# Kernel tuning notes

Hardware: AMD Instinct MI355X
Metric: run time of the kernel (lower is better)

## Reference

```python
import jax, jax.numpy as jnp
import numpy as np

N, M = 2048, 2048
NODE_DIM = 64
HIDDEN_DIM = 64  # must equal NODE_DIM due to broadcast in msg = weights * h_r
LN_EPS = 1e-5


def setup_inputs() -> dict:
    key = jax.random.key(0)
    ks = jax.random.split(key, 14)
    s_edge1 = 1.0 / np.sqrt(4.0)
    s_edge2 = 1.0 / np.sqrt(HIDDEN_DIM)
    s_n1 = 1.0 / np.sqrt(NODE_DIM + HIDDEN_DIM)
    s_n2 = 1.0 / np.sqrt(NODE_DIM)
    return {
        "h_l": jax.random.normal(ks[0], (N, NODE_DIM), jnp.float32),
        "x_l": jax.random.normal(ks[1], (N, 3), jnp.float32),
        "h_r": jax.random.normal(ks[2], (M, NODE_DIM), jnp.float32),
        "x_r": jax.random.normal(ks[3], (M, 3), jnp.float32),
        # edge_mlp: Linear(4, hidden), SiLU, Linear(hidden, hidden)
        "W1": jax.random.uniform(ks[4], (4, HIDDEN_DIM), jnp.float32, -s_edge1, s_edge1),
        "b1": jax.random.uniform(ks[5], (HIDDEN_DIM,), jnp.float32, -s_edge1, s_edge1),
        "W2": jax.random.uniform(ks[6], (HIDDEN_DIM, HIDDEN_DIM), jnp.float32, -s_edge2, s_edge2),
        "b2": jax.random.uniform(ks[7], (HIDDEN_DIM,), jnp.float32, -s_edge2, s_edge2),
        # node_update: Linear(node+hidden, node), LayerNorm(node), SiLU, Linear(node, node)
        "Wn1": jax.random.uniform(ks[8], (NODE_DIM + HIDDEN_DIM, NODE_DIM), jnp.float32, -s_n1, s_n1),
        "bn1": jax.random.uniform(ks[9], (NODE_DIM,), jnp.float32, -s_n1, s_n1),
        "ln_g": jnp.ones((NODE_DIM,), jnp.float32),
        "ln_b": jnp.zeros((NODE_DIM,), jnp.float32),
        "Wn2": jax.random.uniform(ks[10], (NODE_DIM, NODE_DIM), jnp.float32, -s_n2, s_n2),
        "bn2": jax.random.uniform(ks[11], (NODE_DIM,), jnp.float32, -s_n2, s_n2),
    }


def _forward(h_l, x_l, h_r, x_r, W1, b1, W2, b2, Wn1, bn1, ln_g, ln_b, Wn2, bn2):
    # squared pairwise distances [N, M]
    d2 = jnp.sum((x_l[:, None, :] - x_r[None, :, :]) ** 2, axis=-1)
    dist_feat = jnp.exp(-d2 / 5.0)
    # chemical-property interaction matrices from last 3 node features
    l_p, r_p = h_l[:, -3:], h_r[:, -3:]
    hbond = l_p[:, 0:1] * r_p[:, 1:2].T + l_p[:, 1:2] * r_p[:, 0:1].T  # [N, M]
    hydro = l_p[:, 2:3] * r_p[:, 2:3].T                                # [N, M]
    edge_raw = jnp.stack([dist_feat, hbond, hydro, jnp.ones_like(d2)], axis=-1)  # [N, M, 4]
    # edge MLP -> sigmoid gating weights [N, M, H]
    e = jax.nn.silu(edge_raw @ W1 + b1) @ W2 + b2
    w = jax.nn.sigmoid(e)
    # weighted, normalized aggregation over M
    h_agg = jnp.einsum('nmh,mh->nh', w, h_r) / (jnp.sum(w, axis=1) + 1e-6)
    # node update MLP with LayerNorm
    z = jnp.concatenate([h_l, h_agg], axis=-1) @ Wn1 + bn1
    mu = jnp.mean(z, axis=-1, keepdims=True)
    var = jnp.var(z, axis=-1, keepdims=True)
    z = (z - mu) / jnp.sqrt(var + LN_EPS) * ln_g + ln_b
    z = jax.nn.silu(z) @ Wn2 + bn2
    return h_l + z


def reference(h_l, x_l, h_r, x_r, W1, b1, W2, b2, Wn1, bn1, ln_g, ln_b, Wn2, bn2):
    return _forward(h_l, x_l, h_r, x_r, W1, b1, W2, b2, Wn1, bn1, ln_g, ln_b, Wn2, bn2)
```

## Files before the change

kernel.cpp:

```cpp
#include <hip/hip_runtime.h>
#include <hip/hip_bf16.h>
#include <hip/hip_fp16.h>


#define NTOT 2048
#define MTOT 2048
#define MSPLIT 32
#define MCHUNK 64
#define NODE_ROWS 4

typedef _Float16 f16x8 __attribute__((ext_vector_type(8)));
typedef float f32x4  __attribute__((ext_vector_type(4)));
typedef float f32x2  __attribute__((ext_vector_type(2)));
typedef int   i32x4  __attribute__((ext_vector_type(4)));

#define NL2E (-1.4426950408889634f)
#define C1E  (-0.2885390081777927f)

__device__ __forceinline__ float fast_exp2(float x) {
#if __has_builtin(__builtin_amdgcn_exp2f)
  return __builtin_amdgcn_exp2f(x);
#else
  return __exp2f(x);
#endif
}
__device__ __forceinline__ float fast_rcp(float x) {
#if __has_builtin(__builtin_amdgcn_rcpf)
  return __builtin_amdgcn_rcpf(x);
#else
  return 1.0f / x;
#endif
}
__device__ __forceinline__ float fast_rsq(float x) {
#if __has_builtin(__builtin_amdgcn_rsqf)
  return __builtin_amdgcn_rsqf(x);
#else
  return rsqrtf(x);
#endif
}
__device__ __forceinline__ f32x2 pk_fma(f32x2 a, f32x2 b, f32x2 c) {
  return __builtin_elementwise_fma(a, b, c);
}

__device__ __forceinline__ unsigned pack_f16_rtz(float lo, float hi) {
#if __has_builtin(__builtin_amdgcn_cvt_pkrtz)
  auto p = __builtin_amdgcn_cvt_pkrtz(lo, hi);
  return __builtin_bit_cast(unsigned, p);
#else
  union { _Float16 h; unsigned short u; } a, b;
  a.h = (_Float16)lo; b.h = (_Float16)hi;
  return (unsigned)a.u | ((unsigned)b.u << 16);
#endif
}

__global__ __launch_bounds__(256, 2)
void edge_kernel(const float* __restrict__ h_l,
                 const float* __restrict__ x_l,
                 const float* __restrict__ h_r,
                 const float* __restrict__ x_r,
                 const float* __restrict__ W1,
                 const float* __restrict__ b1,
                 const float* __restrict__ W2,
                 const float* __restrict__ b2,
                 float* __restrict__ num_g,
                 float* __restrict__ den_g) {
  __shared__ float hrT[MCHUNK][64];
  __shared__ float xr_s[MCHUNK][8];

  const int tid  = threadIdx.x;
  const int wave = tid >> 6;
  const int lane = tid & 63;
  const int l15  = lane & 15;
  const int quad = lane >> 4;

  const int nblk   = blockIdx.x / MSPLIT;
  const int msplit = blockIdx.x % MSPLIT;
  const int n0     = nblk * 64 + wave * 16;
  const int mBase  = msplit * MCHUNK;

  const int nA = n0 + l15;
  const float xl0 = x_l[nA * 3 + 0];
  const float xl1 = x_l[nA * 3 + 1];
  const float xl2 = x_l[nA * 3 + 2];
  const float slC = fmaf(xl2, xl2, fmaf(xl1, xl1, xl0 * xl0)) * C1E;
  const float lp0 = h_l[nA * 64 + 61];
  const float lp1 = h_l[nA * 64 + 62];
  const float lp2 = h_l[nA * 64 + 63];

  f32x2 w1d2[8], w1h2[8], w1y2[8], b1p2[8];
#pragma unroll
  for (int p = 0; p < 8; ++p) {
    const int j0 = 2 * p, j1 = 2 * p + 1;
    const int hA = (j0 < 8) ? (quad * 8 + j0) : (32 + quad * 8 + (j0 - 8));
    const int hB = (j1 < 8) ? (quad * 8 + j1) : (32 + quad * 8 + (j1 - 8));
    w1d2[p] = f32x2{W1[0 * 64 + hA], W1[0 * 64 + hB]};
    w1h2[p] = f32x2{W1[1 * 64 + hA], W1[1 * 64 + hB]};
    w1y2[p] = f32x2{W1[2 * 64 + hA], W1[2 * 64 + hB]};
    b1p2[p] = f32x2{b1[hA] + W1[3 * 64 + hA], b1[hB] + W1[3 * 64 + hB]};
  }

  f16x8 Bfrag[4][2];
#pragma unroll
  for (int c = 0; c < 4; ++c) {
#pragma unroll
    for (int h = 0; h < 2; ++h) {
      f16x8 f;
#pragma unroll
      for (int j = 0; j < 8; ++j) {
        const int k = h * 32 + quad * 8 + j;
        f[j] = (_Float16)W2[k * 64 + c * 16 + l15];
      }
      Bfrag[c][h] = f;
    }
  }

  f32x2 b2c2[4];
#pragma unroll
  for (int c = 0; c < 4; ++c) {
    const float v = NL2E * b2[c * 16 + l15];
    b2c2[c] = f32x2{v, v};
  }

  for (int idx = tid; idx < MCHUNK * 64; idx += 256) {
    const int mm = idx >> 6, w = idx & 63;
    const int i = w >> 2, c = w & 3;
    hrT[mm][w] = h_r[(mBase + mm) * 64 + c * 16 + i];
  }
  if (tid < MCHUNK) {
    const int m = mBase + tid;
    const float a0 = x_r[m * 3 + 0], a1 = x_r[m * 3 + 1], a2 = x_r[m * 3 + 2];
    const float r0 = h_r[m * 64 + 61], r1 = h_r[m * 64 + 62], r2 = h_r[m * 64 + 63];
    xr_s[tid][0] = a0 * (-2.0f * C1E);
    xr_s[tid][1] = a1 * (-2.0f * C1E);
    xr_s[tid][2] = a2 * (-2.0f * C1E);
    xr_s[tid][3] = fmaf(a2, a2, fmaf(a1, a1, a0 * a0)) * C1E;
    xr_s[tid][4] = r0;
    xr_s[tid][5] = r1;
    xr_s[tid][6] = r2;
    xr_s[tid][7] = 0.f;
  }

  const f32x4 zero4 = {0.f, 0.f, 0.f, 0.f};
  const f32x2 one2 = {1.f, 1.f};
  const f32x2 nl2e2 = {NL2E, NL2E};
  f32x2 numr2[4][2], denr2[4][2];
#pragma unroll
  for (int c = 0; c < 4; ++c)
#pragma unroll
    for (int h = 0; h < 2; ++h) {
      numr2[c][h] = f32x2{0.f, 0.f};
      denr2[c][h] = f32x2{0.f, 0.f};
    }

  __syncthreads();

#pragma unroll 2
  for (int ms = 0; ms < MCHUNK; ++ms) {
    const f32x4 xa = *(const f32x4*)&xr_s[ms][0];
    const f32x4 xb = *(const f32x4*)&xr_s[ms][4];
    const float arg = fmaf(xl0, xa[0], fmaf(xl1, xa[1], fmaf(xl2, xa[2], slC + xa[3])));
    const float dist = fast_exp2(arg);
    const float hb = fmaf(lp0, xb[1], lp1 * xb[0]);
    const float hy = lp2 * xb[2];
    const f32x2 distv = {dist, dist};
    const f32x2 hbv = {hb, hb};
    const f32x2 hyv = {hy, hy};

    f32x2 s2[8];
#pragma unroll
    for (int p = 0; p < 8; ++p) {
      const f32x2 t2 = pk_fma(distv, w1d2[p],
                       pk_fma(hbv, w1h2[p],
                       pk_fma(hyv, w1y2[p], b1p2[p])));
      const f32x2 a2 = t2 * nl2e2;
      f32x2 e2;
      e2.x = fast_exp2(a2.x);
      e2.y = fast_exp2(a2.y);
      const f32x2 dd = e2 + one2;
      f32x2 r2;
      r2.x = fast_rcp(dd.x);
      r2.y = fast_rcp(dd.y);
      s2[p] = t2 * r2;
    }
    i32x4 p0, p1;
    p0.x = pack_f16_rtz(s2[0].x, s2[0].y);  p0.y = pack_f16_rtz(s2[1].x, s2[1].y);
    p0.z = pack_f16_rtz(s2[2].x, s2[2].y);  p0.w = pack_f16_rtz(s2[3].x, s2[3].y);
    p1.x = pack_f16_rtz(s2[4].x, s2[4].y);  p1.y = pack_f16_rtz(s2[5].x, s2[5].y);
    p1.z = pack_f16_rtz(s2[6].x, s2[6].y);  p1.w = pack_f16_rtz(s2[7].x, s2[7].y);
    const f16x8 A0 = __builtin_bit_cast(f16x8, p0);
    const f16x8 A1 = __builtin_bit_cast(f16x8, p1);

    f32x4 acc[4];
#pragma unroll
    for (int c = 0; c < 4; ++c) {
      acc[c] = __builtin_amdgcn_mfma_f32_16x16x32_f16(A0, Bfrag[c][0], zero4, 0, 0, 0);
      acc[c] = __builtin_amdgcn_mfma_f32_16x16x32_f16(A1, Bfrag[c][1], acc[c], 0, 0, 0);
    }

    const f32x4 hrv4 = *(const f32x4*)&hrT[ms][l15 * 4];
#pragma unroll
    for (int c = 0; c < 4; ++c) {
      const f32x2 hrv2 = {hrv4[c], hrv4[c]};
#pragma unroll
      for (int h = 0; h < 2; ++h) {
        const f32x2 a2 = {acc[c][2 * h], acc[c][2 * h + 1]};
        const f32x2 arg2 = pk_fma(a2, nl2e2, b2c2[c]);
        f32x2 e2;
        e2.x = fast_exp2(arg2.x);
        e2.y = fast_exp2(arg2.y);
        const f32x2 dden = e2 + one2;
        f32x2 w2;
        w2.x = fast_rcp(dden.x);
        w2.y = fast_rcp(dden.y);
        numr2[c][h] = pk_fma(w2, hrv2, numr2[c][h]);
        denr2[c][h] = denr2[c][h] + w2;
      }
    }
  }

#pragma unroll
  for (int c = 0; c < 4; ++c)
#pragma unroll
    for (int h = 0; h < 2; ++h)
#pragma unroll
      for (int k = 0; k < 2; ++k) {
        const int r = 2 * h + k;
        const int n = n0 + quad * 4 + r;
        const int h2 = c * 16 + l15;
        atomicAdd(&num_g[n * 64 + h2], k ? numr2[c][h].y : numr2[c][h].x);
        atomicAdd(&den_g[n * 64 + h2], k ? denr2[c][h].y : denr2[c][h].x);
      }
}

__global__ __launch_bounds__(256)
void node_kernel(const float* __restrict__ h_l,
                 const float* __restrict__ num_g,
                 const float* __restrict__ den_g,
                 const float* __restrict__ Wn1,
                 const float* __restrict__ bn1,
                 const float* __restrict__ ln_g,
                 const float* __restrict__ ln_b,
                 const float* __restrict__ Wn2,
                 const float* __restrict__ bn2,
                 float* __restrict__ out) {
  __shared__ float Wn1_s[128 * 64];
  __shared__ float Wn2_s[64 * 64];
  __shared__ float xbuf[4][128];
  __shared__ float zbuf[4][64];

  const int tid = threadIdx.x;
  for (int i = tid; i < 128 * 64; i += 256) Wn1_s[i] = Wn1[i];
  for (int i = tid; i < 64 * 64; i += 256) Wn2_s[i] = Wn2[i];

  const int wave = tid >> 6, lane = tid & 63;

  __syncthreads();

#pragma unroll 1
  for (int it = 0; it < NODE_ROWS / 4; ++it) {
    const int row = blockIdx.x * NODE_ROWS + it * 4 + wave;

    const float hl = h_l[row * 64 + lane];
    const float dn = den_g[row * 64 + lane] + 1e-6f;
    const float hagg = num_g[row * 64 + lane] * fast_rcp(dn);
    xbuf[wave][lane] = hl;
    xbuf[wave][64 + lane] = hagg;

    float t = bn1[lane];
#pragma unroll 8
    for (int k = 0; k < 128; ++k) t = fmaf(xbuf[wave][k], Wn1_s[k * 64 + lane], t);

    float s1 = t, s2 = t * t;
#pragma unroll
    for (int off = 32; off; off >>= 1) {
      s1 += __shfl_xor(s1, off);
      s2 += __shfl_xor(s2, off);
    }
    const float mu = s1 * 0.015625f;
    const float var = fmaf(s2, 0.015625f, -mu * mu);
    const float rs = fast_rsq(var + 1e-5f);
    const float zn = fmaf((t - mu) * rs, ln_g[lane], ln_b[lane]);
    const float sz = zn * fast_rcp(1.0f + fast_exp2(zn * NL2E));
    zbuf[wave][lane] = sz;

    float o = bn2[lane];
#pragma unroll 8
    for (int k = 0; k < 64; ++k) o = fmaf(zbuf[wave][k], Wn2_s[k * 64 + lane], o);

    out[row * 64 + lane] = hl + o;
  }
}

extern "C" void kernel_launch(void* const* d_in, const int* in_sizes, int n_in,
                              void* d_out, int out_size, void* d_ws, size_t ws_size,
                              hipStream_t stream) {
  const float* h_l = (const float*)d_in[0];
  const float* x_l = (const float*)d_in[1];
  const float* h_r = (const float*)d_in[2];
  const float* x_r = (const float*)d_in[3];
  const float* W1  = (const float*)d_in[4];
  const float* b1  = (const float*)d_in[5];
  const float* W2  = (const float*)d_in[6];
  const float* b2  = (const float*)d_in[7];
  const float* Wn1 = (const float*)d_in[8];
  const float* bn1 = (const float*)d_in[9];
  const float* lng = (const float*)d_in[10];
  const float* lnb = (const float*)d_in[11];
  const float* Wn2 = (const float*)d_in[12];
  const float* bn2 = (const float*)d_in[13];

  float* num_g = (float*)d_ws;
  float* den_g = num_g + (size_t)NTOT * 64;

  hipMemsetAsync(d_ws, 0, (size_t)NTOT * 64 * 2 * sizeof(float), stream);
  edge_kernel<<<dim3((NTOT / 64) * MSPLIT), dim3(256), 0, stream>>>(
      h_l, x_l, h_r, x_r, W1, b1, W2, b2, num_g, den_g);
  node_kernel<<<dim3(NTOT / NODE_ROWS), dim3(256), 0, stream>>>(
      h_l, num_g, den_g, Wn1, bn1, lng, lnb, Wn2, bn2, (float*)d_out);
}
```

Measured before the change: 214.7 us.

## Fuse node update into edge kernel via last-block-done counter

Merges the node-update kernel into the edge kernel. Each N-block's split blocks bump a global atomic counter, and the last one to finish runs the node MLP for its 64 rows, reading Wn1/Wn2 straight from global memory instead of staging them in shared memory. This removes one kernel launch and the separate pass over num/den. In exchange, only 32 blocks do the node work, serially over 16 rows per wave, which can lengthen the tail.

```diff
diff --git a/kernel.cpp b/kernel.cpp
--- a/kernel.cpp
+++ b/kernel.cpp
@@ -7,7 +7,6 @@
 #define MTOT 2048
 #define MSPLIT 32
 #define MCHUNK 64
-#define NODE_ROWS 4
 
 typedef _Float16 f16x8 __attribute__((ext_vector_type(8)));
 typedef float f32x4  __attribute__((ext_vector_type(4)));
@@ -16,6 +15,8 @@
 
 #define NL2E (-1.4426950408889634f)
 #define C1E  (-0.2885390081777927f)
+
+__device__ unsigned g_cnt[NTOT / 64];
 
 __device__ __forceinline__ float fast_exp2(float x) {
 #if __has_builtin(__builtin_amdgcn_exp2f)
@@ -54,18 +55,28 @@
 }
 
 __global__ __launch_bounds__(256, 2)
-void edge_kernel(const float* __restrict__ h_l,
-                 const float* __restrict__ x_l,
-                 const float* __restrict__ h_r,
-                 const float* __restrict__ x_r,
-                 const float* __restrict__ W1,
-                 const float* __restrict__ b1,
-                 const float* __restrict__ W2,
-                 const float* __restrict__ b2,
-                 float* __restrict__ num_g,
-                 float* __restrict__ den_g) {
+void fused_kernel(const float* __restrict__ h_l,
+                  const float* __restrict__ x_l,
+                  const float* __restrict__ h_r,
+                  const float* __restrict__ x_r,
+                  const float* __restrict__ W1,
+                  const float* __restrict__ b1,
+                  const float* __restrict__ W2,
+                  const float* __restrict__ b2,
+                  const float* __restrict__ Wn1,
+                  const float* __restrict__ bn1,
+                  const float* __restrict__ ln_g,
+                  const float* __restrict__ ln_b,
+                  const float* __restrict__ Wn2,
+                  const float* __restrict__ bn2,
+                  float* num_g,
+                  float* den_g,
+                  float* __restrict__ out) {
   __shared__ float hrT[MCHUNK][64];
   __shared__ float xr_s[MCHUNK][8];
+  __shared__ float xbuf[4][128];
+  __shared__ float zbuf[4][64];
+  __shared__ unsigned last_flag;
 
   const int tid  = threadIdx.x;
   const int wave = tid >> 6;
@@ -230,54 +241,51 @@
         atomicAdd(&num_g[n * 64 + h2], k ? numr2[c][h].y : numr2[c][h].x);
         atomicAdd(&den_g[n * 64 + h2], k ? denr2[c][h].y : denr2[c][h].x);
       }
-}
-
-__global__ __launch_bounds__(256)
-void node_kernel(const float* __restrict__ h_l,
-                 const float* __restrict__ num_g,
-                 const float* __restrict__ den_g,
-                 const float* __restrict__ Wn1,
-                 const float* __restrict__ bn1,
-                 const float* __restrict__ ln_g,
-                 const float* __restrict__ ln_b,
-                 const float* __restrict__ Wn2,
-                 const float* __restrict__ bn2,
-                 float* __restrict__ out) {
-  __shared__ float Wn1_s[128 * 64];
-  __shared__ float Wn2_s[64 * 64];
-  __shared__ float xbuf[4][128];
-  __shared__ float zbuf[4][64];
-
-  const int tid = threadIdx.x;
-  for (int i = tid; i < 128 * 64; i += 256) Wn1_s[i] = Wn1[i];
-  for (int i = tid; i < 64 * 64; i += 256) Wn2_s[i] = Wn2[i];
-
-  const int wave = tid >> 6, lane = tid & 63;
-
+
+  __threadfence();
   __syncthreads();
-
+  if (tid == 0) {
+    const unsigned old = __hip_atomic_fetch_add(&g_cnt[nblk], 1u,
+                                                __ATOMIC_ACQ_REL,
+                                                __HIP_MEMORY_SCOPE_AGENT);
+    last_flag = (old == MSPLIT - 1) ? 1u : 0u;
+    if (last_flag) {
+      __hip_atomic_store(&g_cnt[nblk], 0u, __ATOMIC_RELAXED,
+                         __HIP_MEMORY_SCOPE_AGENT);
+    }
+  }
+  __syncthreads();
+  if (!last_flag) return;
+
+  __threadfence();
+  const int rbase = nblk * 64 + wave * 16;
 #pragma unroll 1
-  for (int it = 0; it < NODE_ROWS / 4; ++it) {
-    const int row = blockIdx.x * NODE_ROWS + it * 4 + wave;
+  for (int rr = 0; rr < 16; ++rr) {
+    const int row = rbase + rr;
 
     const float hl = h_l[row * 64 + lane];
-    const float dn = den_g[row * 64 + lane] + 1e-6f;
-    const float hagg = num_g[row * 64 + lane] * fast_rcp(dn);
+    const float nu = __hip_atomic_load(&num_g[row * 64 + lane],
+                                       __ATOMIC_RELAXED,
+                                       __HIP_MEMORY_SCOPE_AGENT);
+    const float de = __hip_atomic_load(&den_g[row * 64 + lane],
+                                       __ATOMIC_RELAXED,
+                                       __HIP_MEMORY_SCOPE_AGENT);
+    const float hagg = nu * fast_rcp(de + 1e-6f);
     xbuf[wave][lane] = hl;
     xbuf[wave][64 + lane] = hagg;
 
     float t = bn1[lane];
 #pragma unroll 8
-    for (int k = 0; k < 128; ++k) t = fmaf(xbuf[wave][k], Wn1_s[k * 64 + lane], t);
-
-    float s1 = t, s2 = t * t;
+    for (int k = 0; k < 128; ++k) t = fmaf(xbuf[wave][k], Wn1[k * 64 + lane], t);
+
+    float s1 = t, s2v = t * t;
 #pragma unroll
     for (int off = 32; off; off >>= 1) {
       s1 += __shfl_xor(s1, off);
-      s2 += __shfl_xor(s2, off);
+      s2v += __shfl_xor(s2v, off);
     }
     const float mu = s1 * 0.015625f;
-    const float var = fmaf(s2, 0.015625f, -mu * mu);
+    const float var = fmaf(s2v, 0.015625f, -mu * mu);
     const float rs = fast_rsq(var + 1e-5f);
     const float zn = fmaf((t - mu) * rs, ln_g[lane], ln_b[lane]);
     const float sz = zn * fast_rcp(1.0f + fast_exp2(zn * NL2E));
@@ -285,7 +293,7 @@
 
     float o = bn2[lane];
 #pragma unroll 8
-    for (int k = 0; k < 64; ++k) o = fmaf(zbuf[wave][k], Wn2_s[k * 64 + lane], o);
+    for (int k = 0; k < 64; ++k) o = fmaf(zbuf[wave][k], Wn2[k * 64 + lane], o);
 
     out[row * 64 + lane] = hl + o;
   }
@@ -313,8 +321,7 @@
   float* den_g = num_g + (size_t)NTOT * 64;
 
   hipMemsetAsync(d_ws, 0, (size_t)NTOT * 64 * 2 * sizeof(float), stream);
-  edge_kernel<<<dim3((NTOT / 64) * MSPLIT), dim3(256), 0, stream>>>(
-      h_l, x_l, h_r, x_r, W1, b1, W2, b2, num_g, den_g);
-  node_kernel<<<dim3(NTOT / NODE_ROWS), dim3(256), 0, stream>>>(
-      h_l, num_g, den_g, Wn1, bn1, lng, lnb, Wn2, bn2, (float*)d_out);
-}
+  fused_kernel<<<dim3((NTOT / 64) * MSPLIT), dim3(256), 0, stream>>>(
+      h_l, x_l, h_r, x_r, W1, b1, W2, b2, Wn1, bn1, lng, lnb, Wn2, bn2,
+      num_g, den_g, (float*)d_out);
+}
```

Result: slower. 340.2 us (+58.5%).
